# Optimization experiments

Measured on AMD Instinct MI355X. Metric: run time of the kernel, lower is better.

The kernel has to match this reference:

```python
import jax, jax.numpy as jnp
import numpy as np

N_DF = 96      # number of deep-filtered frequency bins
BASE = 0       # base_bin
N_ORDER = 5    # FIR taps along time


def setup_inputs() -> dict:
    key = jax.random.key(0)
    k1, k2 = jax.random.split(key)
    B, T, F = 8, 3000, 481
    # complex spectrogram stored as [..., 2] = (real, imag)
    spec = jax.random.normal(k1, (B, T, F, 2), dtype=jnp.float32)
    # per-frame complex FIR coefficients: [..., :N_ORDER]=real, [..., N_ORDER:]=imag
    coef = jax.random.normal(k2, (B, T, N_DF, 2 * N_ORDER), dtype=jnp.float32)
    return {"spec": spec, "coef": coef}


def _df_forward(spec, coef):
    T = spec.shape[1]
    # narrow to the deep-filter band
    xr = spec[:, :, BASE:BASE + N_DF, 0]  # [B,T,N_DF]
    xi = spec[:, :, BASE:BASE + N_DF, 1]
    # causal pad along time (ConstantPad2d((0,0,n_order-1,0)))
    pad = ((0, 0), (N_ORDER - 1, 0), (0, 0))
    pr = jnp.pad(xr, pad)
    pi = jnp.pad(xi, pad)
    # unfold(time, n_order, 1) -> [B,T,N_DF,N_ORDER]; loop is over fixed tap count
    ur = jnp.stack([pr[:, k:k + T] for k in range(N_ORDER)], axis=-1)
    ui = jnp.stack([pi[:, k:k + T] for k in range(N_ORDER)], axis=-1)
    cr = coef[..., :N_ORDER]
    ci = coef[..., N_ORDER:]
    # complex sliding dot product: sum_k u[k] * c[k]
    fr = jnp.sum(ur * cr - ui * ci, axis=-1)  # [B,T,N_DF]
    fi = jnp.sum(ur * ci + ui * cr, axis=-1)
    out = spec.at[:, :, BASE:BASE + N_DF, 0].set(fr)
    out = out.at[:, :, BASE:BASE + N_DF, 1].set(fi)
    return out


def reference(spec, coef):
    return _df_forward(spec, coef)
```

## Files before the change

kernel.cpp:

```cpp
#include <hip/hip_runtime.h>


#define BN    8
#define TN    3000
#define FN    481
#define NDF   96
#define NORD  5
#define ROWF  (FN * 2)
#define THALF (TN / 2)

typedef float f2 __attribute__((ext_vector_type(2)));

__global__ __launch_bounds__(256) void copy_kernel(const float4* __restrict__ in,
                                                   float4* __restrict__ out,
                                                   int n4) {
    const int base = blockIdx.x * (256 * 4) + threadIdx.x;
    #pragma unroll
    for (int k = 0; k < 4; ++k) {
        const int idx = base + k * 256;
        if (idx < n4) out[idx] = in[idx];
    }
}

__global__ __launch_bounds__(256) void df_filt_kernel(const float* __restrict__ spec,
                                                      const float* __restrict__ coef,
                                                      float* __restrict__ out) {
    const int i = blockIdx.x * blockDim.x + threadIdx.x;
    const int nFiltP = BN * THALF * NDF;
    if (i >= nFiltP) return;

    const int f   = i % NDF;
    const int bth = i / NDF;
    const int th  = bth % THALF;
    const int b   = bth / THALF;
    const int t0  = th * 2;
    const int bt0   = b * TN + t0;
    const int base0 = bt0 * ROWF + f * 2;

    const f2* cp = (const f2*)(coef + (bt0 * NDF + f) * (2 * NORD));
    const f2* cq = cp + NDF * NORD;
    const f2 c0a = cp[0], c0b = cp[1], c0c = cp[2], c0d = cp[3], c0e = cp[4];
    const f2 c1a = cq[0], c1b = cq[1], c1c = cq[2], c1d = cq[3], c1e = cq[4];

    const float* sp = spec + base0;
    f2 x0, x1, x2, x3, x4, x5;
    if (t0 >= NORD - 1) {
        x0 = *(const f2*)(sp - 4 * ROWF);
        x1 = *(const f2*)(sp - 3 * ROWF);
        x2 = *(const f2*)(sp - 2 * ROWF);
        x3 = *(const f2*)(sp - 1 * ROWF);
        x4 = *(const f2*)(sp);
        x5 = *(const f2*)(sp + 1 * ROWF);
    } else {
        const f2 z = {0.f, 0.f};
        x0 = (t0 >= 4) ? *(const f2*)(sp - 4 * ROWF) : z;
        x1 = (t0 >= 3) ? *(const f2*)(sp - 3 * ROWF) : z;
        x2 = (t0 >= 2) ? *(const f2*)(sp - 2 * ROWF) : z;
        x3 = (t0 >= 1) ? *(const f2*)(sp - 1 * ROWF) : z;
        x4 = *(const f2*)(sp);
        x5 = *(const f2*)(sp + 1 * ROWF);
    }

    float fr0, fi0, fr1, fi1;
    {
        const float cr0 = c0a.x, cr1 = c0a.y, cr2 = c0b.x, cr3 = c0b.y, cr4 = c0c.x;
        const float ci0 = c0c.y, ci1 = c0d.x, ci2 = c0d.y, ci3 = c0e.x, ci4 = c0e.y;
        fr0 = x0.x*cr0 - x0.y*ci0; fi0 = x0.x*ci0 + x0.y*cr0;
        fr0 += x1.x*cr1 - x1.y*ci1; fi0 += x1.x*ci1 + x1.y*cr1;
        fr0 += x2.x*cr2 - x2.y*ci2; fi0 += x2.x*ci2 + x2.y*cr2;
        fr0 += x3.x*cr3 - x3.y*ci3; fi0 += x3.x*ci3 + x3.y*cr3;
        fr0 += x4.x*cr4 - x4.y*ci4; fi0 += x4.x*ci4 + x4.y*cr4;
    }
    {
        const float cr0 = c1a.x, cr1 = c1a.y, cr2 = c1b.x, cr3 = c1b.y, cr4 = c1c.x;
        const float ci0 = c1c.y, ci1 = c1d.x, ci2 = c1d.y, ci3 = c1e.x, ci4 = c1e.y;
        fr1 = x1.x*cr0 - x1.y*ci0; fi1 = x1.x*ci0 + x1.y*cr0;
        fr1 += x2.x*cr1 - x2.y*ci1; fi1 += x2.x*ci1 + x2.y*cr1;
        fr1 += x3.x*cr2 - x3.y*ci2; fi1 += x3.x*ci2 + x3.y*cr2;
        fr1 += x4.x*cr3 - x4.y*ci3; fi1 += x4.x*ci3 + x4.y*cr3;
        fr1 += x5.x*cr4 - x5.y*ci4; fi1 += x5.x*ci4 + x5.y*cr4;
    }

    *(f2*)(out + base0)        = (f2){fr0, fi0};
    *(f2*)(out + base0 + ROWF) = (f2){fr1, fi1};
}

extern "C" void kernel_launch(void* const* d_in, const int* in_sizes, int n_in,
                              void* d_out, int out_size, void* d_ws, size_t ws_size,
                              hipStream_t stream) {
    const float* spec = (const float*)d_in[0];
    const float* coef = (const float*)d_in[1];
    float* out = (float*)d_out;

    const int n4 = BN * TN * FN * 2 / 4;
    const int gridA = (n4 + 1024 - 1) / 1024;
    copy_kernel<<<gridA, 256, 0, stream>>>((const float4*)spec, (float4*)out, n4);

    const int nFiltP = BN * THALF * NDF;
    const int gridB = (nFiltP + 255) / 256;
    df_filt_kernel<<<gridB, 256, 0, stream>>>(spec, coef, out);
}
```

Measured before the change: 227.1 us.

## Fuse passthrough copy and deep filter into one interleaved kernel

Merges the full-spectrum copy and the filter into one launch. Copy blocks move only the bins outside the deep-filter band, using float4 accesses with per-row parity offsets plus a small edge fix-up, so the band that the filter overwrites is no longer copied. Copy and filter blocks are interleaved 2:3 in the grid so both run concurrently, which removes one launch and the redundant traffic for the band. The cost is more complex index arithmetic and hardcoded block counts that must divide the problem exactly.

```diff
diff --git a/kernel.cpp b/kernel.cpp
--- a/kernel.cpp
+++ b/kernel.cpp
@@ -8,81 +8,115 @@
 #define NORD  5
 #define ROWF  (FN * 2)
 #define THALF (TN / 2)
+#define NROWS (BN * TN)
+#define RPB   8
+#define NPB   (NROWS / RPB)
+#define NFB   ((BN * THALF * NDF) / 256)
 
 typedef float f2 __attribute__((ext_vector_type(2)));
 
-__global__ __launch_bounds__(256) void copy_kernel(const float4* __restrict__ in,
-                                                   float4* __restrict__ out,
-                                                   int n4) {
-    const int base = blockIdx.x * (256 * 4) + threadIdx.x;
-    #pragma unroll
-    for (int k = 0; k < 4; ++k) {
-        const int idx = base + k * 256;
-        if (idx < n4) out[idx] = in[idx];
+__global__ __launch_bounds__(256) void df_kernel(const float* __restrict__ spec,
+                                                 const float* __restrict__ coef,
+                                                 float* __restrict__ out) {
+    const int tid = threadIdx.x;
+    const int m   = blockIdx.x % 5;
+
+    if (m < 2) {
+        const int p  = (blockIdx.x / 5) * 2 + m;
+        const int r0 = p * RPB;
+        const float4* in4  = (const float4*)spec;
+        float4*       out4 = (float4*)out;
+
+        int a0, a1, a2, a3, a4, a5;
+        #define PASS_ADDR(j, dst)                                         \
+            {                                                             \
+                const int L  = tid + (j) * 256;                           \
+                const int rl = L / 192;                                   \
+                const int k  = L - rl * 192;                              \
+                const int r  = r0 + rl;                                   \
+                const int q0 = (ROWF * r + ((r & 1) ? 194 : 192)) >> 2;   \
+                dst = q0 + k;                                             \
+            }
+        PASS_ADDR(0, a0) PASS_ADDR(1, a1) PASS_ADDR(2, a2)
+        PASS_ADDR(3, a3) PASS_ADDR(4, a4) PASS_ADDR(5, a5)
+        #undef PASS_ADDR
+
+        const float4 x0 = in4[a0];
+        const float4 x1 = in4[a1];
+        const float4 x2 = in4[a2];
+        const float4 x3 = in4[a3];
+        const float4 x4 = in4[a4];
+        const float4 x5 = in4[a5];
+
+        f2 e; int eidx = 0;
+        if (tid < RPB) {
+            const int r = r0 + tid;
+            eidx = ROWF * r + ((r & 1) ? 192 : 960);
+            e = *(const f2*)(spec + eidx);
+        }
+
+        out4[a0] = x0; out4[a1] = x1; out4[a2] = x2;
+        out4[a3] = x3; out4[a4] = x4; out4[a5] = x5;
+        if (tid < RPB) *(f2*)(out + eidx) = e;
+    } else {
+        const int q = (blockIdx.x / 5) * 3 + (m - 2);
+        const int i = q * 256 + tid;
+
+        const int f   = i % NDF;
+        const int bth = i / NDF;
+        const int th  = bth % THALF;
+        const int b   = bth / THALF;
+        const int t0  = th * 2;
+        const int bt0   = b * TN + t0;
+        const int base0 = bt0 * ROWF + f * 2;
+
+        const f2* cp = (const f2*)(coef + (bt0 * NDF + f) * (2 * NORD));
+        const f2* cq = cp + NDF * NORD;
+        const f2 c0a = cp[0], c0b = cp[1], c0c = cp[2], c0d = cp[3], c0e = cp[4];
+        const f2 c1a = cq[0], c1b = cq[1], c1c = cq[2], c1d = cq[3], c1e = cq[4];
+
+        const float* sp = spec + base0;
+        f2 x0, x1, x2, x3, x4, x5;
+        if (t0 >= NORD - 1) {
+            x0 = *(const f2*)(sp - 4 * ROWF);
+            x1 = *(const f2*)(sp - 3 * ROWF);
+            x2 = *(const f2*)(sp - 2 * ROWF);
+            x3 = *(const f2*)(sp - 1 * ROWF);
+            x4 = *(const f2*)(sp);
+            x5 = *(const f2*)(sp + 1 * ROWF);
+        } else {
+            const f2 z = {0.f, 0.f};
+            x0 = (t0 >= 4) ? *(const f2*)(sp - 4 * ROWF) : z;
+            x1 = (t0 >= 3) ? *(const f2*)(sp - 3 * ROWF) : z;
+            x2 = (t0 >= 2) ? *(const f2*)(sp - 2 * ROWF) : z;
+            x3 = (t0 >= 1) ? *(const f2*)(sp - 1 * ROWF) : z;
+            x4 = *(const f2*)(sp);
+            x5 = *(const f2*)(sp + 1 * ROWF);
+        }
+
+        float fr0, fi0, fr1, fi1;
+        {
+            const float cr0 = c0a.x, cr1 = c0a.y, cr2 = c0b.x, cr3 = c0b.y, cr4 = c0c.x;
+            const float ci0 = c0c.y, ci1 = c0d.x, ci2 = c0d.y, ci3 = c0e.x, ci4 = c0e.y;
+            fr0 = x0.x*cr0 - x0.y*ci0; fi0 = x0.x*ci0 + x0.y*cr0;
+            fr0 += x1.x*cr1 - x1.y*ci1; fi0 += x1.x*ci1 + x1.y*cr1;
+            fr0 += x2.x*cr2 - x2.y*ci2; fi0 += x2.x*ci2 + x2.y*cr2;
+            fr0 += x3.x*cr3 - x3.y*ci3; fi0 += x3.x*ci3 + x3.y*cr3;
+            fr0 += x4.x*cr4 - x4.y*ci4; fi0 += x4.x*ci4 + x4.y*cr4;
+        }
+        {
+            const float cr0 = c1a.x, cr1 = c1a.y, cr2 = c1b.x, cr3 = c1b.y, cr4 = c1c.x;
+            const float ci0 = c1c.y, ci1 = c1d.x, ci2 = c1d.y, ci3 = c1e.x, ci4 = c1e.y;
+            fr1 = x1.x*cr0 - x1.y*ci0; fi1 = x1.x*ci0 + x1.y*cr0;
+            fr1 += x2.x*cr1 - x2.y*ci1; fi1 += x2.x*ci1 + x2.y*cr1;
+            fr1 += x3.x*cr2 - x3.y*ci2; fi1 += x3.x*ci2 + x3.y*cr2;
+            fr1 += x4.x*cr3 - x4.y*ci3; fi1 += x4.x*ci3 + x4.y*cr3;
+            fr1 += x5.x*cr4 - x5.y*ci4; fi1 += x5.x*ci4 + x5.y*cr4;
+        }
+
+        *(f2*)(out + base0)        = (f2){fr0, fi0};
+        *(f2*)(out + base0 + ROWF) = (f2){fr1, fi1};
     }
-}
-
-__global__ __launch_bounds__(256) void df_filt_kernel(const float* __restrict__ spec,
-                                                      const float* __restrict__ coef,
-                                                      float* __restrict__ out) {
-    const int i = blockIdx.x * blockDim.x + threadIdx.x;
-    const int nFiltP = BN * THALF * NDF;
-    if (i >= nFiltP) return;
-
-    const int f   = i % NDF;
-    const int bth = i / NDF;
-    const int th  = bth % THALF;
-    const int b   = bth / THALF;
-    const int t0  = th * 2;
-    const int bt0   = b * TN + t0;
-    const int base0 = bt0 * ROWF + f * 2;
-
-    const f2* cp = (const f2*)(coef + (bt0 * NDF + f) * (2 * NORD));
-    const f2* cq = cp + NDF * NORD;
-    const f2 c0a = cp[0], c0b = cp[1], c0c = cp[2], c0d = cp[3], c0e = cp[4];
-    const f2 c1a = cq[0], c1b = cq[1], c1c = cq[2], c1d = cq[3], c1e = cq[4];
-
-    const float* sp = spec + base0;
-    f2 x0, x1, x2, x3, x4, x5;
-    if (t0 >= NORD - 1) {
-        x0 = *(const f2*)(sp - 4 * ROWF);
-        x1 = *(const f2*)(sp - 3 * ROWF);
-        x2 = *(const f2*)(sp - 2 * ROWF);
-        x3 = *(const f2*)(sp - 1 * ROWF);
-        x4 = *(const f2*)(sp);
-        x5 = *(const f2*)(sp + 1 * ROWF);
-    } else {
-        const f2 z = {0.f, 0.f};
-        x0 = (t0 >= 4) ? *(const f2*)(sp - 4 * ROWF) : z;
-        x1 = (t0 >= 3) ? *(const f2*)(sp - 3 * ROWF) : z;
-        x2 = (t0 >= 2) ? *(const f2*)(sp - 2 * ROWF) : z;
-        x3 = (t0 >= 1) ? *(const f2*)(sp - 1 * ROWF) : z;
-        x4 = *(const f2*)(sp);
-        x5 = *(const f2*)(sp + 1 * ROWF);
-    }
-
-    float fr0, fi0, fr1, fi1;
-    {
-        const float cr0 = c0a.x, cr1 = c0a.y, cr2 = c0b.x, cr3 = c0b.y, cr4 = c0c.x;
-        const float ci0 = c0c.y, ci1 = c0d.x, ci2 = c0d.y, ci3 = c0e.x, ci4 = c0e.y;
-        fr0 = x0.x*cr0 - x0.y*ci0; fi0 = x0.x*ci0 + x0.y*cr0;
-        fr0 += x1.x*cr1 - x1.y*ci1; fi0 += x1.x*ci1 + x1.y*cr1;
-        fr0 += x2.x*cr2 - x2.y*ci2; fi0 += x2.x*ci2 + x2.y*cr2;
-        fr0 += x3.x*cr3 - x3.y*ci3; fi0 += x3.x*ci3 + x3.y*cr3;
-        fr0 += x4.x*cr4 - x4.y*ci4; fi0 += x4.x*ci4 + x4.y*cr4;
-    }
-    {
-        const float cr0 = c1a.x, cr1 = c1a.y, cr2 = c1b.x, cr3 = c1b.y, cr4 = c1c.x;
-        const float ci0 = c1c.y, ci1 = c1d.x, ci2 = c1d.y, ci3 = c1e.x, ci4 = c1e.y;
-        fr1 = x1.x*cr0 - x1.y*ci0; fi1 = x1.x*ci0 + x1.y*cr0;
-        fr1 += x2.x*cr1 - x2.y*ci1; fi1 += x2.x*ci1 + x2.y*cr1;
-        fr1 += x3.x*cr2 - x3.y*ci2; fi1 += x3.x*ci2 + x3.y*cr2;
-        fr1 += x4.x*cr3 - x4.y*ci3; fi1 += x4.x*ci3 + x4.y*cr3;
-        fr1 += x5.x*cr4 - x5.y*ci4; fi1 += x5.x*ci4 + x5.y*cr4;
-    }
-
-    *(f2*)(out + base0)        = (f2){fr0, fi0};
-    *(f2*)(out + base0 + ROWF) = (f2){fr1, fi1};
 }
 
 extern "C" void kernel_launch(void* const* d_in, const int* in_sizes, int n_in,
@@ -92,11 +126,6 @@
     const float* coef = (const float*)d_in[1];
     float* out = (float*)d_out;
 
-    const int n4 = BN * TN * FN * 2 / 4;
-    const int gridA = (n4 + 1024 - 1) / 1024;
-    copy_kernel<<<gridA, 256, 0, stream>>>((const float4*)spec, (float4*)out, n4);
-
-    const int nFiltP = BN * THALF * NDF;
-    const int gridB = (nFiltP + 255) / 256;
-    df_filt_kernel<<<gridB, 256, 0, stream>>>(spec, coef, out);
+    const int grid = NPB + NFB;
+    df_kernel<<<grid, 256, 0, stream>>>(spec, coef, out);
 }
```

New measurement: 227.1 us. Within noise of the previous version (+0.0%).
